# Performance work log

Hardware: AMD Instinct MI355X
Metric: run time of the kernel (lower is better)

## Reference

```python
import jax, jax.numpy as jnp
import numpy as np

BLOCK_SIZE = 32
BLOCK_COUNTS = 4
NEG = -1e9
SEQ_LENS = np.array([512, 384, 448, 256], dtype=np.int64)


def setup_inputs():
    key = jax.random.key(0)
    ks = jax.random.split(key, 5)
    T = int(SEQ_LENS.sum()); H = 4; D = 64
    offs = np.concatenate([[0], np.cumsum(SEQ_LENS)]).astype(np.int64)
    return {
        "q": jax.random.normal(ks[0], (T, H, D), jnp.float32),
        "k": jax.random.normal(ks[1], (T, H, D), jnp.float32),
        "v": jax.random.normal(ks[2], (T, H, D), jnp.float32),
        "g_cmp": jax.random.uniform(ks[3], (T, H), jnp.float32),
        "g_slc": jax.random.uniform(ks[4], (T, H), jnp.float32),
        "x_offsets": jnp.asarray(offs),
    }


def _silu(x):
    return x * jax.nn.sigmoid(x)


def _forward(q, k, v, g_cmp, g_slc, offs):
    bs = BLOCK_SIZE
    B = len(offs) - 1
    seq_lens = offs[1:] - offs[:-1]              # np [B]
    T, H, D = q.shape
    max_n = int(seq_lens.max())
    nb = (max_n + bs - 1) // bs                  # max compressed blocks
    L = nb * bs                                  # padded length (multiple of bs)
    batch_ids = np.repeat(np.arange(B), seq_lens)
    local_ids = np.arange(T) - offs[:-1][batch_ids]

    def pad(x):  # jagged [T, ...] -> padded [B, L, ...]
        return jnp.zeros((B, L) + x.shape[1:], x.dtype).at[batch_ids, local_ids].set(x)

    pq, pk, pv = pad(q), pad(k), pad(v)
    # block-pooled (mean) compressed K/V; partial blocks also divided by bs, as in torch
    k_cmp = pk.reshape(B, nb, bs, H, D).sum(axis=2) / bs   # [B, nb, H, D]
    v_cmp = pv.reshape(B, nb, bs, H, D).sum(axis=2) / bs

    scale = D ** -0.5
    pos = np.arange(max_n)                       # local query positions
    qblk = pos // bs
    blk = np.arange(nb)
    causal = qblk[:, None] >= blk[None, :]       # [max_n, nb]
    seq_valid = pos[None, :] < seq_lens[:, None]  # [B, max_n]
    cmp_lens = (seq_lens + bs - 1) // bs
    blk_valid = blk[None, :] < cmp_lens[:, None]  # [B, nb]

    pq_m = pq[:, :max_n]                          # [B, max_n, H, D]
    scores = jnp.einsum('bqhd,bkhd->bhqk', pq_m, k_cmp) * scale  # [B,H,max_n,nb]

    # --- compressed branch: mask to -1e9, SiLU, zero masked (matches cmp kernel) ---
    m_full = (jnp.asarray(causal)[None, None]
              & jnp.asarray(seq_valid)[:, None, :, None]
              & jnp.asarray(blk_valid)[:, None, None, :])
    m_zero = jnp.asarray(causal)[None, None] & jnp.asarray(blk_valid)[:, None, None, :]
    p_cmp = jnp.where(m_zero, _silu(jnp.where(m_full, scores, NEG)), 0.0)
    o_cmp_pad = jnp.einsum('bhqk,bkhd->bqhd', p_cmp, v_cmp)
    o_cmp_pad = o_cmp_pad * pad(g_cmp)[:, :max_n, :, None]
    o_cmp = o_cmp_pad[batch_ids, local_ids]       # back to jagged [T,H,D]

    # --- per-token top-S block selection on causally masked compressed scores ---
    sel_scores = jnp.where(jnp.asarray(causal)[None, None], scores, -jnp.inf)
    S = min(BLOCK_COUNTS, nb)
    _, topk = jax.lax.top_k(sel_scores, S)        # [B,H,max_n,S] block ids

    # --- selected branch: gather raw K/V from the chosen blocks ---
    r = np.arange(bs)
    tpos = topk[..., None] * bs + r               # [B,H,max_n,S,bs] local key pos < L
    pk_h = pk.transpose(0, 2, 1, 3)               # [B,H,L,D]
    pv_h = pv.transpose(0, 2, 1, 3)
    idx = tpos.reshape(B, H, -1)
    k_sel = jnp.take_along_axis(pk_h, idx[..., None], axis=2).reshape(B, H, max_n, S, bs, D)
    v_sel = jnp.take_along_axis(pv_h, idx[..., None], axis=2).reshape(B, H, max_n, S, bs, D)
    pq_h = pq_m.transpose(0, 2, 1, 3)             # [B,H,max_n,D]
    s_slc = jnp.einsum('bhmd,bhmsrd->bhmsr', pq_h, k_sel) * scale
    within = tpos < jnp.asarray(seq_lens)[:, None, None, None, None]
    caus = tpos <= jnp.asarray(pos)[None, None, :, None, None]
    p_slc = jnp.where(within & caus, _silu(s_slc), 0.0)
    o_slc_pad = jnp.einsum('bhmsr,bhmsrd->bmhd', p_slc, v_sel)
    o_slc_pad = o_slc_pad * pad(g_slc)[:, :max_n, :, None]
    o_slc = o_slc_pad[batch_ids, local_ids]
    return o_cmp, o_slc


def reference(q, k, v, g_cmp, g_slc, x_offsets):
    return _forward(q, k, v, g_cmp, g_slc, np.asarray(x_offsets))
```

## Files before the change

### kernel.cpp

```cpp
#include <hip/hip_runtime.h>
#include <math.h>

#define HH 4
#define DD 64
#define BS 32
#define SSEL 4
#define STRIDE (HH * DD)

typedef __attribute__((ext_vector_type(8))) short bf16x8;
typedef __attribute__((ext_vector_type(4))) float f32x4;

__device__ __forceinline__ float silu_f(float x) { return x / (1.0f + __expf(-x)); }

__device__ __forceinline__ unsigned short f2bf(float f) {
    unsigned int x = __float_as_uint(f);
    return (unsigned short)((x + 0x7FFFu + ((x >> 16) & 1u)) >> 16);
}
__device__ __forceinline__ unsigned int pk2bf(float a, float b) {
    return (unsigned int)f2bf(a) | ((unsigned int)f2bf(b) << 16);
}

__global__ __launch_bounds__(512) void nsa_all(
        const float* __restrict__ q, const float* __restrict__ k,
        const float* __restrict__ v, const float* __restrict__ gc,
        const float* __restrict__ gs, const int* __restrict__ offs,
        int B, int T, float* __restrict__ out) {
    __shared__ float Qf[32][68];
    __shared__ float Kc[16][68];
    __shared__ float Vc[16][64];
    __shared__ float Sc[32][17];
    __shared__ float Ps[32][17];
    __shared__ unsigned char selb[32][16];
    __shared__ unsigned int  Msk[32];
    __shared__ unsigned short Qs[32][64];
    __shared__ unsigned short Ks[8][32][64];
    __shared__ unsigned int   Pw[8][32][20];
    __shared__ float          Op[4][32][68];

    int qbh = blockIdx.x;
    int h   = qbh & (HH - 1);
    int qb  = qbh / HH;

    int b = -1, lb = 0, cum = 0, off = 0, n = 0;
    for (int i = 0; i < B; ++i) {
        int o0 = offs[i], o1 = offs[i + 1];
        int nbi = (o1 - o0 + BS - 1) / BS;
        if (qb < cum + nbi) { b = i; lb = qb - cum; off = o0; n = o1 - o0; break; }
        cum += nbi;
    }
    if (b < 0) return;
    int t0  = off + lb * BS;
    int nbl = lb + 1;
    const float scale = 0.125f;
    int tid = threadIdx.x;
    int w = tid >> 6, lane = tid & 63;
    int l15 = lane & 15, g = lane >> 4;

    int krow = lane >> 1, khf = lane & 1;
    float4 K0[8], K1[8];
    float  tv0[4][8], tv1[4][8];
    bool have0 = (w <= lb);
    bool have1 = (w + 8 <= lb);
    if (have0) {
        const float4* kp = (const float4*)(k + (size_t)(off + w * BS + krow) * STRIDE
                                           + h * DD + khf * 32);
        #pragma unroll
        for (int cc = 0; cc < 8; ++cc) K0[cc] = kp[cc];
        const float* vg = v + (size_t)(off + w * BS) * STRIDE + h * DD;
        #pragma unroll
        for (int dt = 0; dt < 4; ++dt)
            #pragma unroll
            for (int j = 0; j < 8; ++j)
                tv0[dt][j] = vg[(size_t)(g * 8 + j) * STRIDE + dt * 16 + l15];
    }
    if (have1) {
        const float4* kp = (const float4*)(k + (size_t)(off + (w + 8) * BS + krow) * STRIDE
                                           + h * DD + khf * 32);
        #pragma unroll
        for (int cc = 0; cc < 8; ++cc) K1[cc] = kp[cc];
        const float* vg = v + (size_t)(off + (w + 8) * BS) * STRIDE + h * DD;
        #pragma unroll
        for (int dt = 0; dt < 4; ++dt)
            #pragma unroll
            for (int j = 0; j < 8; ++j)
                tv1[dt][j] = vg[(size_t)(g * 8 + j) * STRIDE + dt * 16 + l15];
    }

    {
        int row = tid >> 4, dg = tid & 15;
        int trow = min(t0 + row, T - 1);
        float4 a = *(const float4*)(q + (size_t)trow * STRIDE + h * DD + dg * 4);
        a.x *= scale; a.y *= scale; a.z *= scale; a.w *= scale;
        *(float4*)&Qf[row][dg * 4] = a;
        uint2 uu = { pk2bf(a.x, a.y), pk2bf(a.z, a.w) };
        *(uint2*)&Qs[row][(((dg >> 1) ^ (row & 7)) * 8) + (dg & 1) * 4] = uu;
    }

    for (int idx = tid; idx < nbl * 64; idx += 512) {
        int j = idx >> 6, d = idx & 63;
        const float* kp = k + (size_t)(off + j * BS) * STRIDE + h * DD + d;
        const float* vp = v + (size_t)(off + j * BS) * STRIDE + h * DD + d;
        float ks = 0.f, vs = 0.f;
        #pragma unroll
        for (int r = 0; r < BS; ++r) {
            ks += kp[(size_t)r * STRIDE];
            vs += vp[(size_t)r * STRIDE];
        }
        Kc[j][d] = ks * (1.f / BS);
        Vc[j][d] = vs * (1.f / BS);
    }
    __syncthreads();

    {
        int qq = tid >> 4, j = tid & 15;
        if (j < nbl) {
            float s = 0.f;
            #pragma unroll
            for (int i = 0; i < 16; ++i) {
                float4 qv = *(float4*)&Qf[qq][i * 4];
                float4 kk = *(float4*)&Kc[j][i * 4];
                s += qv.x * kk.x + qv.y * kk.y + qv.z * kk.z + qv.w * kk.w;
            }
            Sc[qq][j] = s;
        }
    }
    __syncthreads();

    {
        int qq = tid >> 4, j = tid & 15;
        if (j < nbl) {
            float sj = Sc[qq][j];
            int rank = 0;
            for (int i = 0; i < nbl; ++i) {
                float si = Sc[qq][i];
                rank += (si > sj) || (si == sj && i < j);
            }
            selb[qq][j] = (unsigned char)(rank < SSEL);
            Ps[qq][j]   = silu_f(sj);
        } else {
            selb[qq][j] = 0;
        }
    }
    __syncthreads();

    if (tid < 32) {
        unsigned int m = 0;
        #pragma unroll
        for (int j = 0; j < 16; ++j) m |= ((unsigned int)selb[tid][j]) << j;
        Msk[tid] = m;
    }
    {
        int qq = tid >> 4, dg = tid & 15;
        float4 o = {0.f, 0.f, 0.f, 0.f};
        for (int blk = 0; blk < nbl; ++blk) {
            float p = Ps[qq][blk];
            float4 vv = *(float4*)&Vc[blk][dg * 4];
            o.x += p * vv.x; o.y += p * vv.y; o.z += p * vv.z; o.w += p * vv.w;
        }
        if (lb * BS + qq < n) {
            float gv = gc[(size_t)(t0 + qq) * HH + h];
            o.x *= gv; o.y *= gv; o.z *= gv; o.w *= gv;
            *(float4*)(out + (size_t)(t0 + qq) * STRIDE + h * DD + dg * 4) = o;
        }
    }
    __syncthreads();

    unsigned int Msq[2];
    Msq[0] = Msk[l15];
    Msq[1] = Msk[16 + l15];

    f32x4 oacc[4][2];
    #pragma unroll
    for (int dt = 0; dt < 4; ++dt)
        #pragma unroll
        for (int qt = 0; qt < 2; ++qt)
            oacc[dt][qt] = (f32x4){0.f, 0.f, 0.f, 0.f};

#define SLC_STEP(KB, KX, TV)                                                          \
    {                                                                                 \
        const int kb = (KB);                                                          \
                                   \
        _Pragma("unroll")                                                             \
        for (int cc = 0; cc < 4; ++cc) {                                              \
            float4 x = KX[cc * 2], y = KX[cc * 2 + 1];                                \
            uint4 uu;                                                                 \
            uu.x = pk2bf(x.x, x.y); uu.y = pk2bf(x.z, x.w);                           \
            uu.z = pk2bf(y.x, y.y); uu.w = pk2bf(y.z, y.w);                           \
            int c = khf * 4 + cc;                                                     \
            *(uint4*)&Ks[w][krow][(c ^ (krow & 7)) * 8] = uu;                         \
        }                                                                             \
                                                       \
        bf16x8 a1[2][2], b1[2][2];                                                    \
        _Pragma("unroll")                                                             \
        for (int ds = 0; ds < 2; ++ds)                                                \
            _Pragma("unroll")                                                         \
            for (int tt = 0; tt < 2; ++tt) {                                          \
                a1[tt][ds] = *(bf16x8*)&Ks[w][tt * 16 + l15][((g + ds * 4) ^ (l15 & 7)) * 8]; \
                b1[tt][ds] = *(bf16x8*)&Qs[tt * 16 + l15][((g + ds * 4) ^ (l15 & 7)) * 8];    \
            }                                                                         \
        f32x4 s[2][2];                                                                \
        _Pragma("unroll")                                                             \
        for (int kt = 0; kt < 2; ++kt)                                                \
            _Pragma("unroll")                                                         \
            for (int qt = 0; qt < 2; ++qt) {                                          \
                s[kt][qt] = (f32x4){0.f, 0.f, 0.f, 0.f};                              \
                s[kt][qt] = __builtin_amdgcn_mfma_f32_16x16x32_bf16(a1[kt][0], b1[qt][0], s[kt][qt], 0, 0, 0); \
                s[kt][qt] = __builtin_amdgcn_mfma_f32_16x16x32_bf16(a1[kt][1], b1[qt][1], s[kt][qt], 0, 0, 0); \
            }                                                                         \
                                                     \
        _Pragma("unroll")                                                             \
        for (int kt = 0; kt < 2; ++kt)                                                \
            _Pragma("unroll")                                                         \
            for (int qt = 0; qt < 2; ++qt) {                                          \
                bool selbit = (Msq[qt] >> kb) & 1u;                                   \
                float pv[4];                                                          \
                _Pragma("unroll")                                                     \
                for (int r = 0; r < 4; ++r) {                                         \
                    int k_l = kt * 16 + g * 4 + r;                                    \
                    int q_l = qt * 16 + l15;                                          \
                    bool ok = selbit && (kb < lb || k_l <= q_l);                      \
                    pv[r] = ok ? silu_f(s[kt][qt][r]) : 0.f;                          \
                }                                                                     \
                Pw[w][qt * 16 + l15][kt * 8 + g * 2 + 0] = pk2bf(pv[0], pv[1]);       \
                Pw[w][qt * 16 + l15][kt * 8 + g * 2 + 1] = pk2bf(pv[2], pv[3]);       \
            }                                                                         \
        bf16x8 b2[2];                                                                 \
        b2[0] = *(bf16x8*)&Pw[w][l15][g * 4];                                         \
        b2[1] = *(bf16x8*)&Pw[w][16 + l15][g * 4];                                    \
        bf16x8 a2[4];                                                                 \
        _Pragma("unroll")                                                             \
        for (int dt = 0; dt < 4; ++dt) {                                              \
            union { unsigned int u[4]; bf16x8 v8; } cu;                               \
            cu.u[0] = pk2bf(TV[dt][0], TV[dt][1]);                                    \
            cu.u[1] = pk2bf(TV[dt][2], TV[dt][3]);                                    \
            cu.u[2] = pk2bf(TV[dt][4], TV[dt][5]);                                    \
            cu.u[3] = pk2bf(TV[dt][6], TV[dt][7]);                                    \
            a2[dt] = cu.v8;                                                           \
        }                                                                             \
        _Pragma("unroll")                                                             \
        for (int dt = 0; dt < 4; ++dt)                                                \
            _Pragma("unroll")                                                         \
            for (int qt = 0; qt < 2; ++qt)                                            \
                oacc[dt][qt] = __builtin_amdgcn_mfma_f32_16x16x32_bf16(a2[dt], b2[qt], oacc[dt][qt], 0, 0, 0); \
    }

    if (have0) SLC_STEP(w, K0, tv0)
    if (have1) SLC_STEP(w + 8, K1, tv1)
#undef SLC_STEP

    if (w < 4) {
        #pragma unroll
        for (int dt = 0; dt < 4; ++dt)
            #pragma unroll
            for (int qt = 0; qt < 2; ++qt)
                #pragma unroll
                for (int r = 0; r < 4; ++r)
                    Op[w][qt * 16 + l15][dt * 16 + g * 4 + r] = oacc[dt][qt][r];
    }
    __syncthreads();
    if (w >= 4) {
        #pragma unroll
        for (int dt = 0; dt < 4; ++dt)
            #pragma unroll
            for (int qt = 0; qt < 2; ++qt)
                #pragma unroll
                for (int r = 0; r < 4; ++r)
                    Op[w - 4][qt * 16 + l15][dt * 16 + g * 4 + r] += oacc[dt][qt][r];
    }
    __syncthreads();

    {
        int qq = tid >> 4, dg = tid & 15;
        if (lb * BS + qq < n) {
            float gv = gs[(size_t)(t0 + qq) * HH + h];
            float o[4];
            #pragma unroll
            for (int i = 0; i < 4; ++i) {
                int d = dg * 4 + i;
                o[i] = (Op[0][qq][d] + Op[1][qq][d] + Op[2][qq][d] + Op[3][qq][d]) * gv;
            }
            *(float4*)(out + (size_t)T * STRIDE + (size_t)(t0 + qq) * STRIDE + h * DD + dg * 4)
                = (float4){o[0], o[1], o[2], o[3]};
        }
    }
}

extern "C" void kernel_launch(void* const* d_in, const int* in_sizes, int n_in,
                              void* d_out, int out_size, void* d_ws, size_t ws_size,
                              hipStream_t stream) {
    const float* q    = (const float*)d_in[0];
    const float* k    = (const float*)d_in[1];
    const float* v    = (const float*)d_in[2];
    const float* gc   = (const float*)d_in[3];
    const float* gs   = (const float*)d_in[4];
    const int*   offs = (const int*)d_in[5];

    int B = in_sizes[5] - 1;
    int T = out_size / (2 * STRIDE);
    int nbcap  = (T + BS - 1) / BS;
    int nqbcap = nbcap + B;

    nsa_all<<<dim3((unsigned)(nqbcap * HH)), dim3(512), 0, stream>>>(
        q, k, v, gc, gs, offs, B, T, (float*)d_out);
}
```

Before: 20.70 us.

## Defer second key-block loads to overlap with first block compute, vectorize pooling

The second selected K/V block is no longer loaded up front. It is now prefetched after the first block is packed, so the load overlaps the first block's MFMA work, which cuts peak register pressure. The launch bounds now request 2 blocks per CU. Block mean-pooling now uses float4 loads, with separate threads for K and V. The risks are later arrival of the second block's data and register spilling under the tighter occupancy target.

```diff
diff --git a/kernel.cpp b/kernel.cpp
--- a/kernel.cpp
+++ b/kernel.cpp
@@ -20,7 +20,7 @@
     return (unsigned int)f2bf(a) | ((unsigned int)f2bf(b) << 16);
 }
 
-__global__ __launch_bounds__(512) void nsa_all(
+__global__ __launch_bounds__(512, 2) void nsa_all(
         const float* __restrict__ q, const float* __restrict__ k,
         const float* __restrict__ v, const float* __restrict__ gc,
         const float* __restrict__ gs, const int* __restrict__ offs,
@@ -55,10 +55,10 @@
     int tid = threadIdx.x;
     int w = tid >> 6, lane = tid & 63;
     int l15 = lane & 15, g = lane >> 4;
-
     int krow = lane >> 1, khf = lane & 1;
-    float4 K0[8], K1[8];
-    float  tv0[4][8], tv1[4][8];
+
+    float4 K0[8];
+    float  tv0[4][8];
     bool have0 = (w <= lb);
     bool have1 = (w + 8 <= lb);
     if (have0) {
@@ -72,18 +72,6 @@
             #pragma unroll
             for (int j = 0; j < 8; ++j)
                 tv0[dt][j] = vg[(size_t)(g * 8 + j) * STRIDE + dt * 16 + l15];
-    }
-    if (have1) {
-        const float4* kp = (const float4*)(k + (size_t)(off + (w + 8) * BS + krow) * STRIDE
-                                           + h * DD + khf * 32);
-        #pragma unroll
-        for (int cc = 0; cc < 8; ++cc) K1[cc] = kp[cc];
-        const float* vg = v + (size_t)(off + (w + 8) * BS) * STRIDE + h * DD;
-        #pragma unroll
-        for (int dt = 0; dt < 4; ++dt)
-            #pragma unroll
-            for (int j = 0; j < 8; ++j)
-                tv1[dt][j] = vg[(size_t)(g * 8 + j) * STRIDE + dt * 16 + l15];
     }
 
     {
@@ -96,18 +84,18 @@
         *(uint2*)&Qs[row][(((dg >> 1) ^ (row & 7)) * 8) + (dg & 1) * 4] = uu;
     }
 
-    for (int idx = tid; idx < nbl * 64; idx += 512) {
-        int j = idx >> 6, d = idx & 63;
-        const float* kp = k + (size_t)(off + j * BS) * STRIDE + h * DD + d;
-        const float* vp = v + (size_t)(off + j * BS) * STRIDE + h * DD + d;
-        float ks = 0.f, vs = 0.f;
+    if (tid < nbl * 32) {
+        int j = tid >> 5, rest = tid & 31, kind = rest >> 4, d4 = rest & 15;
+        const float* base = (kind ? v : k) + (size_t)(off + j * BS) * STRIDE + h * DD + d4 * 4;
+        float4 acc = {0.f, 0.f, 0.f, 0.f};
         #pragma unroll
         for (int r = 0; r < BS; ++r) {
-            ks += kp[(size_t)r * STRIDE];
-            vs += vp[(size_t)r * STRIDE];
-        }
-        Kc[j][d] = ks * (1.f / BS);
-        Vc[j][d] = vs * (1.f / BS);
+            float4 x = *(const float4*)(base + (size_t)r * STRIDE);
+            acc.x += x.x; acc.y += x.y; acc.z += x.z; acc.w += x.w;
+        }
+        acc.x *= (1.f / BS); acc.y *= (1.f / BS); acc.z *= (1.f / BS); acc.w *= (1.f / BS);
+        if (kind) *(float4*)&Vc[j][d4 * 4] = acc;
+        else      *(float4*)&Kc[j][d4 * 4] = acc;
     }
     __syncthreads();
 
@@ -176,77 +164,97 @@
         for (int qt = 0; qt < 2; ++qt)
             oacc[dt][qt] = (f32x4){0.f, 0.f, 0.f, 0.f};
 
-#define SLC_STEP(KB, KX, TV)                                                          \
-    {                                                                                 \
-        const int kb = (KB);                                                          \
-                                   \
-        _Pragma("unroll")                                                             \
-        for (int cc = 0; cc < 4; ++cc) {                                              \
-            float4 x = KX[cc * 2], y = KX[cc * 2 + 1];                                \
-            uint4 uu;                                                                 \
-            uu.x = pk2bf(x.x, x.y); uu.y = pk2bf(x.z, x.w);                           \
-            uu.z = pk2bf(y.x, y.y); uu.w = pk2bf(y.z, y.w);                           \
-            int c = khf * 4 + cc;                                                     \
-            *(uint4*)&Ks[w][krow][(c ^ (krow & 7)) * 8] = uu;                         \
-        }                                                                             \
-                                                       \
-        bf16x8 a1[2][2], b1[2][2];                                                    \
-        _Pragma("unroll")                                                             \
-        for (int ds = 0; ds < 2; ++ds)                                                \
-            _Pragma("unroll")                                                         \
-            for (int tt = 0; tt < 2; ++tt) {                                          \
+#define PACK_K(KX)                                                                     \
+    _Pragma("unroll")                                                                  \
+    for (int cc = 0; cc < 4; ++cc) {                                                   \
+        float4 x = KX[cc * 2], y = KX[cc * 2 + 1];                                     \
+        uint4 uu;                                                                      \
+        uu.x = pk2bf(x.x, x.y); uu.y = pk2bf(x.z, x.w);                                \
+        uu.z = pk2bf(y.x, y.y); uu.w = pk2bf(y.z, y.w);                                \
+        int c = khf * 4 + cc;                                                          \
+        *(uint4*)&Ks[w][krow][(c ^ (krow & 7)) * 8] = uu;                              \
+    }
+
+#define COMPUTE_STEP(KB, TV)                                                           \
+    {                                                                                  \
+        const int kb = (KB);                                                           \
+        bf16x8 a1[2][2], b1[2][2];                                                     \
+        _Pragma("unroll")                                                              \
+        for (int ds = 0; ds < 2; ++ds)                                                 \
+            _Pragma("unroll")                                                          \
+            for (int tt = 0; tt < 2; ++tt) {                                           \
                 a1[tt][ds] = *(bf16x8*)&Ks[w][tt * 16 + l15][((g + ds * 4) ^ (l15 & 7)) * 8]; \
                 b1[tt][ds] = *(bf16x8*)&Qs[tt * 16 + l15][((g + ds * 4) ^ (l15 & 7)) * 8];    \
-            }                                                                         \
-        f32x4 s[2][2];                                                                \
-        _Pragma("unroll")                                                             \
-        for (int kt = 0; kt < 2; ++kt)                                                \
-            _Pragma("unroll")                                                         \
-            for (int qt = 0; qt < 2; ++qt) {                                          \
-                s[kt][qt] = (f32x4){0.f, 0.f, 0.f, 0.f};                              \
+            }                                                                          \
+        f32x4 s[2][2];                                                                 \
+        _Pragma("unroll")                                                              \
+        for (int kt = 0; kt < 2; ++kt)                                                 \
+            _Pragma("unroll")                                                          \
+            for (int qt = 0; qt < 2; ++qt) {                                           \
+                s[kt][qt] = (f32x4){0.f, 0.f, 0.f, 0.f};                               \
                 s[kt][qt] = __builtin_amdgcn_mfma_f32_16x16x32_bf16(a1[kt][0], b1[qt][0], s[kt][qt], 0, 0, 0); \
                 s[kt][qt] = __builtin_amdgcn_mfma_f32_16x16x32_bf16(a1[kt][1], b1[qt][1], s[kt][qt], 0, 0, 0); \
-            }                                                                         \
-                                                     \
-        _Pragma("unroll")                                                             \
-        for (int kt = 0; kt < 2; ++kt)                                                \
-            _Pragma("unroll")                                                         \
-            for (int qt = 0; qt < 2; ++qt) {                                          \
-                bool selbit = (Msq[qt] >> kb) & 1u;                                   \
-                float pv[4];                                                          \
-                _Pragma("unroll")                                                     \
-                for (int r = 0; r < 4; ++r) {                                         \
-                    int k_l = kt * 16 + g * 4 + r;                                    \
-                    int q_l = qt * 16 + l15;                                          \
-                    bool ok = selbit && (kb < lb || k_l <= q_l);                      \
-                    pv[r] = ok ? silu_f(s[kt][qt][r]) : 0.f;                          \
-                }                                                                     \
-                Pw[w][qt * 16 + l15][kt * 8 + g * 2 + 0] = pk2bf(pv[0], pv[1]);       \
-                Pw[w][qt * 16 + l15][kt * 8 + g * 2 + 1] = pk2bf(pv[2], pv[3]);       \
-            }                                                                         \
-        bf16x8 b2[2];                                                                 \
-        b2[0] = *(bf16x8*)&Pw[w][l15][g * 4];                                         \
-        b2[1] = *(bf16x8*)&Pw[w][16 + l15][g * 4];                                    \
-        bf16x8 a2[4];                                                                 \
-        _Pragma("unroll")                                                             \
-        for (int dt = 0; dt < 4; ++dt) {                                              \
-            union { unsigned int u[4]; bf16x8 v8; } cu;                               \
-            cu.u[0] = pk2bf(TV[dt][0], TV[dt][1]);                                    \
-            cu.u[1] = pk2bf(TV[dt][2], TV[dt][3]);                                    \
-            cu.u[2] = pk2bf(TV[dt][4], TV[dt][5]);                                    \
-            cu.u[3] = pk2bf(TV[dt][6], TV[dt][7]);                                    \
-            a2[dt] = cu.v8;                                                           \
-        }                                                                             \
-        _Pragma("unroll")                                                             \
-        for (int dt = 0; dt < 4; ++dt)                                                \
-            _Pragma("unroll")                                                         \
-            for (int qt = 0; qt < 2; ++qt)                                            \
+            }                                                                          \
+        _Pragma("unroll")                                                              \
+        for (int kt = 0; kt < 2; ++kt)                                                 \
+            _Pragma("unroll")                                                          \
+            for (int qt = 0; qt < 2; ++qt) {                                           \
+                bool selbit = (Msq[qt] >> kb) & 1u;                                    \
+                float pv[4];                                                           \
+                _Pragma("unroll")                                                      \
+                for (int r = 0; r < 4; ++r) {                                          \
+                    int k_l = kt * 16 + g * 4 + r;                                     \
+                    int q_l = qt * 16 + l15;                                           \
+                    bool ok = selbit && (kb < lb || k_l <= q_l);                       \
+                    pv[r] = ok ? silu_f(s[kt][qt][r]) : 0.f;                           \
+                }                                                                      \
+                Pw[w][qt * 16 + l15][kt * 8 + g * 2 + 0] = pk2bf(pv[0], pv[1]);        \
+                Pw[w][qt * 16 + l15][kt * 8 + g * 2 + 1] = pk2bf(pv[2], pv[3]);        \
+            }                                                                          \
+        bf16x8 b2[2];                                                                  \
+        b2[0] = *(bf16x8*)&Pw[w][l15][g * 4];                                          \
+        b2[1] = *(bf16x8*)&Pw[w][16 + l15][g * 4];                                     \
+        bf16x8 a2[4];                                                                  \
+        _Pragma("unroll")                                                              \
+        for (int dt = 0; dt < 4; ++dt) {                                               \
+            union { unsigned int u[4]; bf16x8 v8; } cu;                                \
+            cu.u[0] = pk2bf(TV[dt][0], TV[dt][1]);                                     \
+            cu.u[1] = pk2bf(TV[dt][2], TV[dt][3]);                                     \
+            cu.u[2] = pk2bf(TV[dt][4], TV[dt][5]);                                     \
+            cu.u[3] = pk2bf(TV[dt][6], TV[dt][7]);                                     \
+            a2[dt] = cu.v8;                                                            \
+        }                                                                              \
+        _Pragma("unroll")                                                              \
+        for (int dt = 0; dt < 4; ++dt)                                                 \
+            _Pragma("unroll")                                                          \
+            for (int qt = 0; qt < 2; ++qt)                                             \
                 oacc[dt][qt] = __builtin_amdgcn_mfma_f32_16x16x32_bf16(a2[dt], b2[qt], oacc[dt][qt], 0, 0, 0); \
     }
 
-    if (have0) SLC_STEP(w, K0, tv0)
-    if (have1) SLC_STEP(w + 8, K1, tv1)
-#undef SLC_STEP
+    float4 kxn[8];
+    float  tvn[4][8];
+    if (have0) {
+        PACK_K(K0)
+        if (have1) {
+            const float4* kp = (const float4*)(k + (size_t)(off + (w + 8) * BS + krow) * STRIDE
+                                               + h * DD + khf * 32);
+            #pragma unroll
+            for (int cc = 0; cc < 8; ++cc) kxn[cc] = kp[cc];
+            const float* vg = v + (size_t)(off + (w + 8) * BS) * STRIDE + h * DD;
+            #pragma unroll
+            for (int dt = 0; dt < 4; ++dt)
+                #pragma unroll
+                for (int j = 0; j < 8; ++j)
+                    tvn[dt][j] = vg[(size_t)(g * 8 + j) * STRIDE + dt * 16 + l15];
+        }
+        COMPUTE_STEP(w, tv0)
+    }
+    if (have1) {
+        PACK_K(kxn)
+        COMPUTE_STEP(w + 8, tvn)
+    }
+#undef PACK_K
+#undef COMPUTE_STEP
 
     if (w < 4) {
         #pragma unroll
```

Result: faster. 19.60 us (-5.3%).
